# Performance work log

Measured on AMD Instinct MI355X. Metric: run time of the kernel, lower is better.

Reference implementation:

```python
import jax, jax.numpy as jnp
import numpy as np

WINDOW = 20  # local attention window, per create_sparse_mask


def _make_mask(rng, n, sparsity_ratio=0.1):
    # local band: |i - j| <= window//2 (covers start/end clamping and the diagonal)
    idx = jnp.arange(n)
    mask = jnp.abs(idx[:, None] - idx[None, :]) <= (WINDOW // 2)
    # random edges: n_random (i, j) pairs set to 1 (duplicates harmless)
    n_random = int(sparsity_ratio * n * n)
    k1, k2 = jax.random.split(rng)
    ri = jax.random.randint(k1, (n_random,), 0, n)
    rj = jax.random.randint(k2, (n_random,), 0, n)
    mask = mask.at[ri, rj].set(True)
    return mask  # [n, n] bool


def setup_inputs() -> dict:
    rng = jax.random.key(0)
    kq, kk, kv, km = jax.random.split(rng, 4)
    B, H, S, D = 1, 8, 4096, 32
    return {
        "query": jax.random.normal(kq, (B, H, S, D), dtype=jnp.float32),
        "key": jax.random.normal(kk, (B, H, S, D), dtype=jnp.float32),
        "value": jax.random.normal(kv, (B, H, S, D), dtype=jnp.float32),
        "mask": _make_mask(km, S, sparsity_ratio=0.1),
    }


def reference(query, key, value, mask):
    # query/key/value: [B, H, S, D]; mask: [S, S] bool (True = attend)
    head_dim = query.shape[-1]
    scale = 1.0 / jnp.sqrt(jnp.float32(head_dim))
    scores = jnp.einsum("bhqd,bhkd->bhqk", query, key) * scale
    # torch: scores = scores * mask; masked_fill(mask == 0, -inf) -> equivalent to where
    scores = jnp.where(mask[None, None, :, :], scores, -jnp.inf)
    attn = jax.nn.softmax(scores, axis=-1)
    attn = jnp.nan_to_num(attn, nan=0.0)
    return jnp.einsum("bhqk,bhkd->bhqd", attn, value)
```

## Files before the change

### kernel.cpp

```cpp
#include <hip/hip_runtime.h>
#include <hip/hip_bf16.h>


#define S_  4096
#define D_  32
#define H_  8

typedef _Float16 half8 __attribute__((ext_vector_type(8)));
typedef __fp16 fp16x2 __attribute__((ext_vector_type(2)));
typedef short short8 __attribute__((ext_vector_type(8)));
typedef short short4v __attribute__((ext_vector_type(4)));
typedef float float4v __attribute__((ext_vector_type(4)));
typedef unsigned short ushort_t;
typedef unsigned int u32;

#if __has_builtin(__builtin_amdgcn_exp2f)
#define EXP2(x) __builtin_amdgcn_exp2f(x)
#else
#define EXP2(x) exp2f(x)
#endif

__device__ inline ushort_t f2h(float x) {
    union { _Float16 h; ushort_t u; } c; c.h = (_Float16)x; return c.u;
}

__global__ __launch_bounds__(256)
void prep_qkv(const float* __restrict__ Q, const float* __restrict__ K,
              const float* __restrict__ V,
              ushort_t* __restrict__ Qh, ushort_t* __restrict__ Kt,
              ushort_t* __restrict__ Vt)
{
    const int bx = blockIdx.x;
    const int tid = threadIdx.x;
    union U8 { ushort_t u[8]; short8 v; };

    if (bx < 512) {
        const int e0 = (bx * 256 + tid) * 8;
        const float c = 0.17677669529663687f * 1.4426950408889634f;
        float4 a = *(const float4*)(Q + e0);
        float4 b = *(const float4*)(Q + e0 + 4);
        float f[8] = {a.x*c, a.y*c, a.z*c, a.w*c, b.x*c, b.y*c, b.z*c, b.w*c};
        U8 o;
#pragma unroll
        for (int i = 0; i < 8; ++i) o.u[i] = f2h(f[i]);
        *(short8*)(Qh + e0) = o.v;
    } else if (bx < 1024) {
        const int e0 = ((bx - 512) * 256 + tid) * 8;
        const int n = (e0 >> 3) & 15, quad = (e0 >> 7) & 3, t16 = (e0 >> 9) & 3;
        const int kt = (e0 >> 11) & 63, h = e0 >> 17;
        const int krow = kt * 64 + t16 * 16 + n;
        const float* src = K + ((size_t)h * S_ + krow) * D_ + quad * 8;
        float4 a = *(const float4*)src;
        float4 b = *(const float4*)(src + 4);
        float f[8] = {a.x, a.y, a.z, a.w, b.x, b.y, b.z, b.w};
        U8 o;
#pragma unroll
        for (int i = 0; i < 8; ++i) o.u[i] = f2h(f[i]);
        *(short8*)(Kt + e0) = o.v;
    } else {
        const int e0 = ((bx - 1024) * 256 + tid) * 8;
        const int n = (e0 >> 3) & 15, quad = (e0 >> 7) & 3;
        const int dhalf = (e0 >> 9) & 1, khalf = (e0 >> 10) & 1;
        const int kt = (e0 >> 11) & 63, h = e0 >> 17;
        const int d = dhalf * 16 + n;
        const int pbase = khalf * 32 + quad * 8;
        U8 o;
#pragma unroll
        for (int j = 0; j < 8; ++j) {
            int p = pbase + j;
            int krow = kt * 64 + (p & 3) * 16 + (p >> 2);
            o.u[j] = f2h(V[((size_t)h * S_ + krow) * D_ + d]);
        }
        *(short8*)(Vt + e0) = o.v;
    }
}

__global__ __launch_bounds__(256)
void prep_mask(const int* __restrict__ mask, ushort_t* __restrict__ mlane)
{
    __shared__ u32 msh[4096];
    const int tid = threadIdx.x;
    const int mb = blockIdx.x;
    const int qt16 = mb >> 2, cc = mb & 3;
#pragma unroll
    for (int i = 0; i < 16; ++i) {
        int4 m4 = *(const int4*)(mask + (size_t)(qt16 * 16 + i) * S_ + cc * 1024 + tid * 4);
        u32 v = (m4.x != 0 ? 1u : 0u) | (m4.y != 0 ? 0x100u : 0u)
              | (m4.z != 0 ? 0x10000u : 0u) | (m4.w != 0 ? 0x1000000u : 0u);
        msh[i * 256 + tid] = v;
    }
    __syncthreads();
    const int kt_local = tid >> 4, j = tid & 15;
    const int quad = j >> 2, n2 = j & 3;
    u32 o16[4] = {0, 0, 0, 0};
#pragma unroll
    for (int t16 = 0; t16 < 4; ++t16)
#pragma unroll
        for (int reg = 0; reg < 4; ++reg) {
            u32 v = msh[(quad * 4 + reg) * 256 + kt_local * 16 + t16 * 4 + n2];
            const int bp = t16 * 4 + reg;
            o16[0] |= (v & 1u) << bp;
            o16[1] |= ((v >> 8) & 1u) << bp;
            o16[2] |= ((v >> 16) & 1u) << bp;
            o16[3] |= ((v >> 24) & 1u) << bp;
        }
    union { u32 w[2]; short4v s; } pk;
    pk.w[0] = o16[0] | (o16[1] << 16);
    pk.w[1] = o16[2] | (o16[3] << 16);
    const int kt = cc * 16 + kt_local;
    *(short4v*)(mlane + ((size_t)(qt16 * 64 + kt) * 64 + j * 4)) = pk.s;
}


#define PS_STRIDE 72

__device__ inline void gl_lds16(const ushort_t* g, ushort_t* l) {
    __builtin_amdgcn_global_load_lds((const __attribute__((address_space(1))) void*)g,
                                     (__attribute__((address_space(3))) void*)l,
                                     16, 0, 0);
}

__global__ __launch_bounds__(512, 2)
void attn_mfma(const ushort_t* __restrict__ Qh, const ushort_t* __restrict__ Kt,
               const ushort_t* __restrict__ Vt, const ushort_t* __restrict__ mlane,
               float* __restrict__ out)
{
    __shared__ __align__(16) ushort_t sm[16384 + 8 * 16 * PS_STRIDE];
    ushort_t* K_s  = sm;
    ushort_t* Vt_s = sm + 8192;

    const int h  = blockIdx.y;
    const int q0 = blockIdx.x * 64;
    const int tid = threadIdx.x;
    const int w = tid >> 6, l = tid & 63;
    const int half = w >> 2, wl = w & 3;
    const int n16 = l & 15, quad = l >> 4;

    ushort_t* Ps = sm + 16384 + w * 16 * PS_STRIDE;

    const int qt16_u = __builtin_amdgcn_readfirstlane(blockIdx.x * 4 + wl);
    const ushort_t* mlw = mlane + ((size_t)qt16_u << 12);

    const int qrow = q0 + wl * 16 + n16;
    const half8 qh = *(const half8*)(Qh + ((size_t)h * S_ + qrow) * D_ + quad * 8);

    half8 ones;
#pragma unroll
    for (int i = 0; i < 8; ++i) ones[i] = (_Float16)1.0f;

    float4v o0 = {0.f, 0.f, 0.f, 0.f};
    float4v o1 = {0.f, 0.f, 0.f, 0.f};
    float4v lacc = {0.f, 0.f, 0.f, 0.f};

    const int hb = half * 4096;
    const int kt_base = half * 32;

    {
        const size_t tb = ((size_t)(h * 64 + kt_base)) * 2048 + wl * 512 + l * 8;
        gl_lds16(Kt + tb, K_s  + hb + wl * 512);
        gl_lds16(Vt + tb, Vt_s + hb + wl * 512);
    }
    __syncthreads();

    for (int i = 0; i < 32; ++i) {
        const int kt = kt_base + i;
        const int cb = hb + (i & 1) * 2048;
        if (i < 31) {
            const int nb = hb + ((i + 1) & 1) * 2048;
            const size_t tb = ((size_t)(h * 64 + kt + 1)) * 2048 + wl * 512 + l * 8;
            gl_lds16(Kt + tb, K_s  + nb + wl * 512);
            gl_lds16(Vt + tb, Vt_s + nb + wl * 512);
        }

        const u32 ml = mlw[kt * 64 + l];

        float pv[4][4];
#pragma unroll
        for (int t16 = 0; t16 < 4; ++t16) {
            const half8 kb = *(const half8*)(K_s + cb + (t16 * 4 + quad) * 128 + n16 * 8);
            float4v c = {0.f, 0.f, 0.f, 0.f};
            c = __builtin_amdgcn_mfma_f32_16x16x32_f16(qh, kb, c, 0, 0, 0);
#pragma unroll
            for (int reg = 0; reg < 4; ++reg) {
                float e = EXP2(c[reg]);
                pv[t16][reg] = (ml & (1u << (t16 * 4 + reg))) ? e : 0.f;
            }
        }
#pragma unroll
        for (int reg = 0; reg < 4; ++reg) {
            fp16x2 h01 = __builtin_amdgcn_cvt_pkrtz(pv[0][reg], pv[1][reg]);
            fp16x2 h23 = __builtin_amdgcn_cvt_pkrtz(pv[2][reg], pv[3][reg]);
            union { fp16x2 hh[2]; short4v s; } pk;
            pk.hh[0] = h01; pk.hh[1] = h23;
            *(short4v*)(Ps + (quad * 4 + reg) * PS_STRIDE + n16 * 4) = pk.s;
        }
        asm volatile("" ::: "memory");

#pragma unroll
        for (int khalf = 0; khalf < 2; ++khalf) {
            const half8 pa = *(const half8*)(Ps + n16 * PS_STRIDE + khalf * 32 + quad * 8);
            const half8 v0 = *(const half8*)(Vt_s + cb + ((khalf * 2 + 0) * 4 + quad) * 128 + n16 * 8);
            const half8 v1 = *(const half8*)(Vt_s + cb + ((khalf * 2 + 1) * 4 + quad) * 128 + n16 * 8);
            o0 = __builtin_amdgcn_mfma_f32_16x16x32_f16(pa, v0, o0, 0, 0, 0);
            o1 = __builtin_amdgcn_mfma_f32_16x16x32_f16(pa, v1, o1, 0, 0, 0);
            lacc = __builtin_amdgcn_mfma_f32_16x16x32_f16(pa, ones, lacc, 0, 0, 0);
        }

        __syncthreads();
    }

    float* red = (float*)sm;
    const int RSTR = 16 * 33 + 16;
    if (half == 1) {
        float* ro = red + wl * RSTR;
#pragma unroll
        for (int reg = 0; reg < 4; ++reg) {
            const int r = quad * 4 + reg;
            ro[r * 33 + n16]      = o0[reg];
            ro[r * 33 + 16 + n16] = o1[reg];
            if (n16 == 0) ro[16 * 33 + r] = lacc[reg];
        }
    }
    __syncthreads();
    if (half == 0) {
        const float* ro = red + wl * RSTR;
#pragma unroll
        for (int reg = 0; reg < 4; ++reg) {
            const int r = quad * 4 + reg;
            const float inv = 1.0f / (lacc[reg] + ro[16 * 33 + r]);
            const int row = q0 + wl * 16 + r;
            float* orow = out + ((size_t)h * S_ + row) * D_;
            orow[n16]      = (o0[reg] + ro[r * 33 + n16]) * inv;
            orow[16 + n16] = (o1[reg] + ro[r * 33 + 16 + n16]) * inv;
        }
    }
}


#define QT 64
#define KT 64
#define NSUB 4
#define KPT 16

__global__ __launch_bounds__(256, 2)
void sparse_attn_fp32(const float* __restrict__ Q, const float* __restrict__ K,
                      const float* __restrict__ V, const int* __restrict__ mask,
                      float* __restrict__ out)
{
    __shared__ float Ks[KT][D_];
    __shared__ float Vs[KT][D_];
    __shared__ float red_o[NSUB][QT][D_ + 1];
    __shared__ float red_l[NSUB][QT];

    const int h = blockIdx.y;
    const int q0 = blockIdx.x * QT;
    const int tid = threadIdx.x;
    const int ql = tid & 63;
    const int sub = tid >> 6;
    const int q = q0 + ql;
    const float scale = 0.17677669529663687f;

    float4 qreg[8];
    const float4* qrow = (const float4*)(Q + ((size_t)h * S_ + q) * D_);
#pragma unroll
    for (int i = 0; i < 8; ++i) qreg[i] = qrow[i];

    float o[D_];
#pragma unroll
    for (int d = 0; d < D_; ++d) o[d] = 0.f;
    float lsum0 = 0.f;

    const float* Kh = K + (size_t)h * S_ * D_;
    const float* Vh = V + (size_t)h * S_ * D_;

    for (int jt = 0; jt < S_; jt += KT) {
        __syncthreads();
        {
            const float4* gK = (const float4*)(Kh + (size_t)jt * D_);
            const float4* gV = (const float4*)(Vh + (size_t)jt * D_);
            float4* sK = (float4*)&Ks[0][0];
            float4* sV = (float4*)&Vs[0][0];
            sK[tid] = gK[tid]; sK[tid + 256] = gK[tid + 256];
            sV[tid] = gV[tid]; sV[tid + 256] = gV[tid + 256];
        }
        __syncthreads();

        int4 m4[4];
        {
            const int4* mr = (const int4*)(mask + (size_t)q * S_ + jt + sub * KPT);
#pragma unroll
            for (int i = 0; i < 4; ++i) m4[i] = mr[i];
        }
        const int* mb = (const int*)m4;

#pragma unroll
        for (int kk = 0; kk < KPT; ++kk) {
            const int jl = sub * KPT + kk;
            const float4* krow = (const float4*)&Ks[jl][0];
            float s = 0.f;
#pragma unroll
            for (int i = 0; i < 8; ++i) {
                float4 kv = krow[i];
                s += qreg[i].x * kv.x + qreg[i].y * kv.y + qreg[i].z * kv.z + qreg[i].w * kv.w;
            }
            const float p = mb[kk] ? __expf(s * scale) : 0.f;
            lsum0 += p;
            const float4* vrow = (const float4*)&Vs[jl][0];
#pragma unroll
            for (int i = 0; i < 8; ++i) {
                float4 vv = vrow[i];
                o[i * 4 + 0] += p * vv.x;
                o[i * 4 + 1] += p * vv.y;
                o[i * 4 + 2] += p * vv.z;
                o[i * 4 + 3] += p * vv.w;
            }
        }
    }

#pragma unroll
    for (int d = 0; d < D_; ++d) red_o[sub][ql][d] = o[d];
    red_l[sub][ql] = lsum0;
    __syncthreads();

    const int eq = tid & 63;
    const int dg = tid >> 6;
    float acc[8];
#pragma unroll
    for (int i = 0; i < 8; ++i) acc[i] = 0.f;
    float lsum = 0.f;
#pragma unroll
    for (int s2 = 0; s2 < NSUB; ++s2) {
        lsum += red_l[s2][eq];
#pragma unroll
        for (int i = 0; i < 8; ++i) acc[i] += red_o[s2][eq][dg * 8 + i];
    }
    const float inv = 1.0f / lsum;
    float* orow = out + ((size_t)h * S_ + q0 + eq) * D_ + dg * 8;
#pragma unroll
    for (int i = 0; i < 8; ++i) orow[i] = acc[i] * inv;
}


extern "C" void kernel_launch(void* const* d_in, const int* in_sizes, int n_in,
                              void* d_out, int out_size, void* d_ws, size_t ws_size,
                              hipStream_t stream) {
    const float* Q = (const float*)d_in[0];
    const float* K = (const float*)d_in[1];
    const float* V = (const float*)d_in[2];
    const int* mask = (const int*)d_in[3];
    float* out = (float*)d_out;

    const size_t MB = 1024 * 1024;
    if (ws_size < 8 * MB) {
        dim3 grid(S_ / QT, H_);
        sparse_attn_fp32<<<grid, 256, 0, stream>>>(Q, K, V, mask, out);
        return;
    }

    char* ws = (char*)d_ws;
    ushort_t* Qh = (ushort_t*)(ws + 0 * MB);
    ushort_t* Kt = (ushort_t*)(ws + 2 * MB);
    ushort_t* Vt = (ushort_t*)(ws + 4 * MB);
    ushort_t* mlane = (ushort_t*)(ws + 6 * MB);

    prep_qkv<<<1536, 256, 0, stream>>>(Q, K, V, Qh, Kt, Vt);
    prep_mask<<<1024, 256, 0, stream>>>(mask, mlane);

    dim3 grid(S_ / 64, H_);
    attn_mfma<<<grid, 512, 0, stream>>>(Qh, Kt, Vt, mlane, out);
}
```

Baseline: 143.1 us.

## Process two 16-row query tiles per wave to reuse K/V LDS reads

The attention kernel drops from 8 waves to 4 waves per block, and each wave now computes two 16-row query tiles (A and B) against the same K/V fragments read from LDS. Each K and V fragment load therefore feeds twice as many MFMAs, and each wave issues more global-to-LDS copies per tile. Per-wave register use roughly doubles and there are fewer waves available to hide latency. The block still covers 64 query rows, so the grid is unchanged.

```diff
diff --git a/kernel.cpp b/kernel.cpp
--- a/kernel.cpp
+++ b/kernel.cpp
@@ -120,12 +120,12 @@
                                      16, 0, 0);
 }
 
-__global__ __launch_bounds__(512, 2)
+__global__ __launch_bounds__(256, 2)
 void attn_mfma(const ushort_t* __restrict__ Qh, const ushort_t* __restrict__ Kt,
                const ushort_t* __restrict__ Vt, const ushort_t* __restrict__ mlane,
                float* __restrict__ out)
 {
-    __shared__ __align__(16) ushort_t sm[16384 + 8 * 16 * PS_STRIDE];
+    __shared__ __align__(16) ushort_t sm[16384 + 4 * 32 * PS_STRIDE];
     ushort_t* K_s  = sm;
     ushort_t* Vt_s = sm + 8192;
 
@@ -133,32 +133,35 @@
     const int q0 = blockIdx.x * 64;
     const int tid = threadIdx.x;
     const int w = tid >> 6, l = tid & 63;
-    const int half = w >> 2, wl = w & 3;
+    const int g = w & 1, hf = w >> 1;
     const int n16 = l & 15, quad = l >> 4;
 
-    ushort_t* Ps = sm + 16384 + w * 16 * PS_STRIDE;
-
-    const int qt16_u = __builtin_amdgcn_readfirstlane(blockIdx.x * 4 + wl);
-    const ushort_t* mlw = mlane + ((size_t)qt16_u << 12);
-
-    const int qrow = q0 + wl * 16 + n16;
-    const half8 qh = *(const half8*)(Qh + ((size_t)h * S_ + qrow) * D_ + quad * 8);
+    ushort_t* Ps = sm + 16384 + w * 32 * PS_STRIDE;
+
+    const int qt16A = __builtin_amdgcn_readfirstlane(blockIdx.x * 4 + g * 2);
+    const ushort_t* mlwA = mlane + ((size_t)qt16A << 12);
+    const ushort_t* mlwB = mlane + ((size_t)(qt16A + 1) << 12);
+
+    const int qA = q0 + g * 32 + n16;
+    const half8 qhA = *(const half8*)(Qh + ((size_t)h * S_ + qA) * D_ + quad * 8);
+    const half8 qhB = *(const half8*)(Qh + ((size_t)h * S_ + qA + 16) * D_ + quad * 8);
 
     half8 ones;
 #pragma unroll
     for (int i = 0; i < 8; ++i) ones[i] = (_Float16)1.0f;
 
-    float4v o0 = {0.f, 0.f, 0.f, 0.f};
-    float4v o1 = {0.f, 0.f, 0.f, 0.f};
-    float4v lacc = {0.f, 0.f, 0.f, 0.f};
-
-    const int hb = half * 4096;
-    const int kt_base = half * 32;
+    float4v o0A = {0,0,0,0}, o1A = {0,0,0,0}, lA = {0,0,0,0};
+    float4v o0B = {0,0,0,0}, o1B = {0,0,0,0}, lB = {0,0,0,0};
+
+    const int hb = hf * 4096;
+    const int kt_base = hf * 32;
 
     {
-        const size_t tb = ((size_t)(h * 64 + kt_base)) * 2048 + wl * 512 + l * 8;
-        gl_lds16(Kt + tb, K_s  + hb + wl * 512);
-        gl_lds16(Vt + tb, Vt_s + hb + wl * 512);
+        const size_t tb = ((size_t)(h * 64 + kt_base)) * 2048 + g * 1024 + l * 8;
+        gl_lds16(Kt + tb,       K_s  + hb + g * 1024 + l * 8);
+        gl_lds16(Kt + tb + 512, K_s  + hb + g * 1024 + 512 + l * 8);
+        gl_lds16(Vt + tb,       Vt_s + hb + g * 1024 + l * 8);
+        gl_lds16(Vt + tb + 512, Vt_s + hb + g * 1024 + 512 + l * 8);
     }
     __syncthreads();
 
@@ -167,71 +170,94 @@
         const int cb = hb + (i & 1) * 2048;
         if (i < 31) {
             const int nb = hb + ((i + 1) & 1) * 2048;
-            const size_t tb = ((size_t)(h * 64 + kt + 1)) * 2048 + wl * 512 + l * 8;
-            gl_lds16(Kt + tb, K_s  + nb + wl * 512);
-            gl_lds16(Vt + tb, Vt_s + nb + wl * 512);
-        }
-
-        const u32 ml = mlw[kt * 64 + l];
-
-        float pv[4][4];
+            const size_t tb = ((size_t)(h * 64 + kt + 1)) * 2048 + g * 1024 + l * 8;
+            gl_lds16(Kt + tb,       K_s  + nb + g * 1024 + l * 8);
+            gl_lds16(Kt + tb + 512, K_s  + nb + g * 1024 + 512 + l * 8);
+            gl_lds16(Vt + tb,       Vt_s + nb + g * 1024 + l * 8);
+            gl_lds16(Vt + tb + 512, Vt_s + nb + g * 1024 + 512 + l * 8);
+        }
+
+        const u32 mlA = mlwA[kt * 64 + l];
+        const u32 mlB = mlwB[kt * 64 + l];
+
+        float pvA[4][4], pvB[4][4];
 #pragma unroll
         for (int t16 = 0; t16 < 4; ++t16) {
             const half8 kb = *(const half8*)(K_s + cb + (t16 * 4 + quad) * 128 + n16 * 8);
-            float4v c = {0.f, 0.f, 0.f, 0.f};
-            c = __builtin_amdgcn_mfma_f32_16x16x32_f16(qh, kb, c, 0, 0, 0);
+            float4v cA = {0,0,0,0}, cB = {0,0,0,0};
+            cA = __builtin_amdgcn_mfma_f32_16x16x32_f16(qhA, kb, cA, 0, 0, 0);
+            cB = __builtin_amdgcn_mfma_f32_16x16x32_f16(qhB, kb, cB, 0, 0, 0);
 #pragma unroll
             for (int reg = 0; reg < 4; ++reg) {
-                float e = EXP2(c[reg]);
-                pv[t16][reg] = (ml & (1u << (t16 * 4 + reg))) ? e : 0.f;
+                float eA = EXP2(cA[reg]);
+                float eB = EXP2(cB[reg]);
+                pvA[t16][reg] = (mlA & (1u << (t16 * 4 + reg))) ? eA : 0.f;
+                pvB[t16][reg] = (mlB & (1u << (t16 * 4 + reg))) ? eB : 0.f;
             }
         }
 #pragma unroll
         for (int reg = 0; reg < 4; ++reg) {
-            fp16x2 h01 = __builtin_amdgcn_cvt_pkrtz(pv[0][reg], pv[1][reg]);
-            fp16x2 h23 = __builtin_amdgcn_cvt_pkrtz(pv[2][reg], pv[3][reg]);
-            union { fp16x2 hh[2]; short4v s; } pk;
-            pk.hh[0] = h01; pk.hh[1] = h23;
-            *(short4v*)(Ps + (quad * 4 + reg) * PS_STRIDE + n16 * 4) = pk.s;
+            fp16x2 a01 = __builtin_amdgcn_cvt_pkrtz(pvA[0][reg], pvA[1][reg]);
+            fp16x2 a23 = __builtin_amdgcn_cvt_pkrtz(pvA[2][reg], pvA[3][reg]);
+            union { fp16x2 hh[2]; short4v s; } pkA;
+            pkA.hh[0] = a01; pkA.hh[1] = a23;
+            *(short4v*)(Ps + (quad * 4 + reg) * PS_STRIDE + n16 * 4) = pkA.s;
+            fp16x2 b01 = __builtin_amdgcn_cvt_pkrtz(pvB[0][reg], pvB[1][reg]);
+            fp16x2 b23 = __builtin_amdgcn_cvt_pkrtz(pvB[2][reg], pvB[3][reg]);
+            union { fp16x2 hh[2]; short4v s; } pkB;
+            pkB.hh[0] = b01; pkB.hh[1] = b23;
+            *(short4v*)(Ps + (16 + quad * 4 + reg) * PS_STRIDE + n16 * 4) = pkB.s;
         }
         asm volatile("" ::: "memory");
 
 #pragma unroll
         for (int khalf = 0; khalf < 2; ++khalf) {
-            const half8 pa = *(const half8*)(Ps + n16 * PS_STRIDE + khalf * 32 + quad * 8);
+            const half8 paA = *(const half8*)(Ps + n16 * PS_STRIDE + khalf * 32 + quad * 8);
+            const half8 paB = *(const half8*)(Ps + (16 + n16) * PS_STRIDE + khalf * 32 + quad * 8);
             const half8 v0 = *(const half8*)(Vt_s + cb + ((khalf * 2 + 0) * 4 + quad) * 128 + n16 * 8);
             const half8 v1 = *(const half8*)(Vt_s + cb + ((khalf * 2 + 1) * 4 + quad) * 128 + n16 * 8);
-            o0 = __builtin_amdgcn_mfma_f32_16x16x32_f16(pa, v0, o0, 0, 0, 0);
-            o1 = __builtin_amdgcn_mfma_f32_16x16x32_f16(pa, v1, o1, 0, 0, 0);
-            lacc = __builtin_amdgcn_mfma_f32_16x16x32_f16(pa, ones, lacc, 0, 0, 0);
+            o0A = __builtin_amdgcn_mfma_f32_16x16x32_f16(paA, v0, o0A, 0, 0, 0);
+            o1A = __builtin_amdgcn_mfma_f32_16x16x32_f16(paA, v1, o1A, 0, 0, 0);
+            lA  = __builtin_amdgcn_mfma_f32_16x16x32_f16(paA, ones, lA, 0, 0, 0);
+            o0B = __builtin_amdgcn_mfma_f32_16x16x32_f16(paB, v0, o0B, 0, 0, 0);
+            o1B = __builtin_amdgcn_mfma_f32_16x16x32_f16(paB, v1, o1B, 0, 0, 0);
+            lB  = __builtin_amdgcn_mfma_f32_16x16x32_f16(paB, ones, lB, 0, 0, 0);
         }
 
         __syncthreads();
     }
 
     float* red = (float*)sm;
-    const int RSTR = 16 * 33 + 16;
-    if (half == 1) {
-        float* ro = red + wl * RSTR;
+    const int RSTR = 32 * 33 + 32;
+    if (hf == 1) {
+        float* ro = red + g * RSTR;
 #pragma unroll
         for (int reg = 0; reg < 4; ++reg) {
-            const int r = quad * 4 + reg;
-            ro[r * 33 + n16]      = o0[reg];
-            ro[r * 33 + 16 + n16] = o1[reg];
-            if (n16 == 0) ro[16 * 33 + r] = lacc[reg];
+            const int rA = quad * 4 + reg, rB = 16 + rA;
+            ro[rA * 33 + n16]      = o0A[reg];
+            ro[rA * 33 + 16 + n16] = o1A[reg];
+            ro[rB * 33 + n16]      = o0B[reg];
+            ro[rB * 33 + 16 + n16] = o1B[reg];
+            if (n16 == 0) {
+                ro[32 * 33 + rA] = lA[reg];
+                ro[32 * 33 + rB] = lB[reg];
+            }
         }
     }
     __syncthreads();
-    if (half == 0) {
-        const float* ro = red + wl * RSTR;
+    if (hf == 0) {
+        const float* ro = red + g * RSTR;
 #pragma unroll
         for (int reg = 0; reg < 4; ++reg) {
-            const int r = quad * 4 + reg;
-            const float inv = 1.0f / (lacc[reg] + ro[16 * 33 + r]);
-            const int row = q0 + wl * 16 + r;
-            float* orow = out + ((size_t)h * S_ + row) * D_;
-            orow[n16]      = (o0[reg] + ro[r * 33 + n16]) * inv;
-            orow[16 + n16] = (o1[reg] + ro[r * 33 + 16 + n16]) * inv;
+            const int rA = quad * 4 + reg, rB = 16 + rA;
+            const float invA = 1.0f / (lA[reg] + ro[32 * 33 + rA]);
+            const float invB = 1.0f / (lB[reg] + ro[32 * 33 + rB]);
+            float* orA = out + ((size_t)h * S_ + q0 + g * 32 + rA) * D_;
+            float* orB = out + ((size_t)h * S_ + q0 + g * 32 + rB) * D_;
+            orA[n16]      = (o0A[reg] + ro[rA * 33 + n16]) * invA;
+            orA[16 + n16] = (o1A[reg] + ro[rA * 33 + 16 + n16]) * invA;
+            orB[n16]      = (o0B[reg] + ro[rB * 33 + n16]) * invB;
+            orB[16 + n16] = (o1B[reg] + ro[rB * 33 + 16 + n16]) * invB;
         }
     }
 }
@@ -367,5 +393,5 @@
     prep_mask<<<1024, 256, 0, stream>>>(mask, mlane);
 
     dim3 grid(S_ / 64, H_);
-    attn_mfma<<<grid, 512, 0, stream>>>(Qh, Kt, Vt, mlane, out);
-}
+    attn_mfma<<<grid, 256, 0, stream>>>(Qh, Kt, Vt, mlane, out);
+}
```

Result: slower. 147.5 us (+3.1%).

## Fuse fp32-to-fp16 QKV conversion into attention kernel and drop prep pass

Applied to the files above, without the earlier changes.

Removes the separate prep_qkv kernel and the fp16 workspace copies of Q, K and V. The attention kernel now loads fp32 Q/K/V directly, scales and converts Q in registers, and loads each K/V tile into registers one iteration ahead. It converts and stores those tiles to LDS after the PV MFMAs, replacing the async global-to-LDS loads. This saves a launch and a global write/read round-trip, at the cost of reading twice the bytes per tile, strided scalar V gathers, and more register pressure in the inner loop.

```diff
diff --git a/kernel.cpp b/kernel.cpp
--- a/kernel.cpp
+++ b/kernel.cpp
@@ -20,61 +20,6 @@
 #define EXP2(x) exp2f(x)
 #endif
 
-__device__ inline ushort_t f2h(float x) {
-    union { _Float16 h; ushort_t u; } c; c.h = (_Float16)x; return c.u;
-}
-
-__global__ __launch_bounds__(256)
-void prep_qkv(const float* __restrict__ Q, const float* __restrict__ K,
-              const float* __restrict__ V,
-              ushort_t* __restrict__ Qh, ushort_t* __restrict__ Kt,
-              ushort_t* __restrict__ Vt)
-{
-    const int bx = blockIdx.x;
-    const int tid = threadIdx.x;
-    union U8 { ushort_t u[8]; short8 v; };
-
-    if (bx < 512) {
-        const int e0 = (bx * 256 + tid) * 8;
-        const float c = 0.17677669529663687f * 1.4426950408889634f;
-        float4 a = *(const float4*)(Q + e0);
-        float4 b = *(const float4*)(Q + e0 + 4);
-        float f[8] = {a.x*c, a.y*c, a.z*c, a.w*c, b.x*c, b.y*c, b.z*c, b.w*c};
-        U8 o;
-#pragma unroll
-        for (int i = 0; i < 8; ++i) o.u[i] = f2h(f[i]);
-        *(short8*)(Qh + e0) = o.v;
-    } else if (bx < 1024) {
-        const int e0 = ((bx - 512) * 256 + tid) * 8;
-        const int n = (e0 >> 3) & 15, quad = (e0 >> 7) & 3, t16 = (e0 >> 9) & 3;
-        const int kt = (e0 >> 11) & 63, h = e0 >> 17;
-        const int krow = kt * 64 + t16 * 16 + n;
-        const float* src = K + ((size_t)h * S_ + krow) * D_ + quad * 8;
-        float4 a = *(const float4*)src;
-        float4 b = *(const float4*)(src + 4);
-        float f[8] = {a.x, a.y, a.z, a.w, b.x, b.y, b.z, b.w};
-        U8 o;
-#pragma unroll
-        for (int i = 0; i < 8; ++i) o.u[i] = f2h(f[i]);
-        *(short8*)(Kt + e0) = o.v;
-    } else {
-        const int e0 = ((bx - 1024) * 256 + tid) * 8;
-        const int n = (e0 >> 3) & 15, quad = (e0 >> 7) & 3;
-        const int dhalf = (e0 >> 9) & 1, khalf = (e0 >> 10) & 1;
-        const int kt = (e0 >> 11) & 63, h = e0 >> 17;
-        const int d = dhalf * 16 + n;
-        const int pbase = khalf * 32 + quad * 8;
-        U8 o;
-#pragma unroll
-        for (int j = 0; j < 8; ++j) {
-            int p = pbase + j;
-            int krow = kt * 64 + (p & 3) * 16 + (p >> 2);
-            o.u[j] = f2h(V[((size_t)h * S_ + krow) * D_ + d]);
-        }
-        *(short8*)(Vt + e0) = o.v;
-    }
-}
-
 __global__ __launch_bounds__(256)
 void prep_mask(const int* __restrict__ mask, ushort_t* __restrict__ mlane)
 {
@@ -114,15 +59,9 @@
 
 #define PS_STRIDE 72
 
-__device__ inline void gl_lds16(const ushort_t* g, ushort_t* l) {
-    __builtin_amdgcn_global_load_lds((const __attribute__((address_space(1))) void*)g,
-                                     (__attribute__((address_space(3))) void*)l,
-                                     16, 0, 0);
-}
-
 __global__ __launch_bounds__(512, 2)
-void attn_mfma(const ushort_t* __restrict__ Qh, const ushort_t* __restrict__ Kt,
-               const ushort_t* __restrict__ Vt, const ushort_t* __restrict__ mlane,
+void attn_mfma(const float* __restrict__ Qf, const float* __restrict__ Kf,
+               const float* __restrict__ Vf, const ushort_t* __restrict__ mlane,
                float* __restrict__ out)
 {
     __shared__ __align__(16) ushort_t sm[16384 + 8 * 16 * PS_STRIDE];
@@ -135,6 +74,7 @@
     const int w = tid >> 6, l = tid & 63;
     const int half = w >> 2, wl = w & 3;
     const int n16 = l & 15, quad = l >> 4;
+    const int khalf = (wl >> 1) & 1, dhalf = wl & 1;
 
     ushort_t* Ps = sm + 16384 + w * 16 * PS_STRIDE;
 
@@ -142,7 +82,15 @@
     const ushort_t* mlw = mlane + ((size_t)qt16_u << 12);
 
     const int qrow = q0 + wl * 16 + n16;
-    const half8 qh = *(const half8*)(Qh + ((size_t)h * S_ + qrow) * D_ + quad * 8);
+    const float* qp = Qf + ((size_t)h * S_ + qrow) * D_ + quad * 8;
+    const float4 qa = *(const float4*)qp;
+    const float4 qb = *(const float4*)(qp + 4);
+    const float c = 0.17677669529663687f * 1.4426950408889634f;
+    half8 qh;
+    qh[0] = (_Float16)(qa.x * c); qh[1] = (_Float16)(qa.y * c);
+    qh[2] = (_Float16)(qa.z * c); qh[3] = (_Float16)(qa.w * c);
+    qh[4] = (_Float16)(qb.x * c); qh[5] = (_Float16)(qb.y * c);
+    qh[6] = (_Float16)(qb.z * c); qh[7] = (_Float16)(qb.w * c);
 
     half8 ones;
 #pragma unroll
@@ -155,22 +103,48 @@
     const int hb = half * 4096;
     const int kt_base = half * 32;
 
-    {
-        const size_t tb = ((size_t)(h * 64 + kt_base)) * 2048 + wl * 512 + l * 8;
-        gl_lds16(Kt + tb, K_s  + hb + wl * 512);
-        gl_lds16(Vt + tb, Vt_s + hb + wl * 512);
-    }
+    float4 ka, kb4;
+    float vv[8];
+    const float* Kh = Kf + (size_t)h * S_ * D_;
+    const float* Vh = Vf + (size_t)h * S_ * D_;
+    const int vd = dhalf * 16 + n16;
+
+#define LOAD_TILE(ktv)                                                        \
+    {                                                                         \
+        const float* kp = Kh + ((size_t)((ktv) * 64 + wl * 16 + n16)) * D_ + quad * 8; \
+        ka  = *(const float4*)kp;                                             \
+        kb4 = *(const float4*)(kp + 4);                                       \
+        _Pragma("unroll")                                                     \
+        for (int j = 0; j < 8; ++j) {                                         \
+            const int krow = (ktv) * 64 + (j & 3) * 16 + khalf * 8 + quad * 2 + (j >> 2); \
+            vv[j] = Vh[(size_t)krow * D_ + vd];                               \
+        }                                                                     \
+    }
+
+#define STORE_TILE(bufv)                                                      \
+    {                                                                         \
+        union { fp16x2 hh[4]; short8 s; } pk;                                 \
+        pk.hh[0] = __builtin_amdgcn_cvt_pkrtz(ka.x, ka.y);                    \
+        pk.hh[1] = __builtin_amdgcn_cvt_pkrtz(ka.z, ka.w);                    \
+        pk.hh[2] = __builtin_amdgcn_cvt_pkrtz(kb4.x, kb4.y);                  \
+        pk.hh[3] = __builtin_amdgcn_cvt_pkrtz(kb4.z, kb4.w);                  \
+        *(short8*)(K_s + hb + (bufv) * 2048 + wl * 512 + l * 8) = pk.s;       \
+        union { fp16x2 hh[4]; short8 s; } pv2;                                \
+        pv2.hh[0] = __builtin_amdgcn_cvt_pkrtz(vv[0], vv[1]);                 \
+        pv2.hh[1] = __builtin_amdgcn_cvt_pkrtz(vv[2], vv[3]);                 \
+        pv2.hh[2] = __builtin_amdgcn_cvt_pkrtz(vv[4], vv[5]);                 \
+        pv2.hh[3] = __builtin_amdgcn_cvt_pkrtz(vv[6], vv[7]);                 \
+        *(short8*)(Vt_s + hb + (bufv) * 2048 + wl * 512 + l * 8) = pv2.s;     \
+    }
+
+    LOAD_TILE(kt_base);
+    STORE_TILE(0);
     __syncthreads();
 
     for (int i = 0; i < 32; ++i) {
         const int kt = kt_base + i;
         const int cb = hb + (i & 1) * 2048;
-        if (i < 31) {
-            const int nb = hb + ((i + 1) & 1) * 2048;
-            const size_t tb = ((size_t)(h * 64 + kt + 1)) * 2048 + wl * 512 + l * 8;
-            gl_lds16(Kt + tb, K_s  + nb + wl * 512);
-            gl_lds16(Vt + tb, Vt_s + nb + wl * 512);
-        }
+        if (i < 31) LOAD_TILE(kt + 1);
 
         const u32 ml = mlw[kt * 64 + l];
 
@@ -178,11 +152,11 @@
 #pragma unroll
         for (int t16 = 0; t16 < 4; ++t16) {
             const half8 kb = *(const half8*)(K_s + cb + (t16 * 4 + quad) * 128 + n16 * 8);
-            float4v c = {0.f, 0.f, 0.f, 0.f};
-            c = __builtin_amdgcn_mfma_f32_16x16x32_f16(qh, kb, c, 0, 0, 0);
+            float4v cc = {0.f, 0.f, 0.f, 0.f};
+            cc = __builtin_amdgcn_mfma_f32_16x16x32_f16(qh, kb, cc, 0, 0, 0);
 #pragma unroll
             for (int reg = 0; reg < 4; ++reg) {
-                float e = EXP2(c[reg]);
+                float e = EXP2(cc[reg]);
                 pv[t16][reg] = (ml & (1u << (t16 * 4 + reg))) ? e : 0.f;
             }
         }
@@ -197,14 +171,16 @@
         asm volatile("" ::: "memory");
 
 #pragma unroll
-        for (int khalf = 0; khalf < 2; ++khalf) {
-            const half8 pa = *(const half8*)(Ps + n16 * PS_STRIDE + khalf * 32 + quad * 8);
-            const half8 v0 = *(const half8*)(Vt_s + cb + ((khalf * 2 + 0) * 4 + quad) * 128 + n16 * 8);
-            const half8 v1 = *(const half8*)(Vt_s + cb + ((khalf * 2 + 1) * 4 + quad) * 128 + n16 * 8);
+        for (int khf = 0; khf < 2; ++khf) {
+            const half8 pa = *(const half8*)(Ps + n16 * PS_STRIDE + khf * 32 + quad * 8);
+            const half8 v0 = *(const half8*)(Vt_s + cb + ((khf * 2 + 0) * 4 + quad) * 128 + n16 * 8);
+            const half8 v1 = *(const half8*)(Vt_s + cb + ((khf * 2 + 1) * 4 + quad) * 128 + n16 * 8);
             o0 = __builtin_amdgcn_mfma_f32_16x16x32_f16(pa, v0, o0, 0, 0, 0);
             o1 = __builtin_amdgcn_mfma_f32_16x16x32_f16(pa, v1, o1, 0, 0, 0);
             lacc = __builtin_amdgcn_mfma_f32_16x16x32_f16(pa, ones, lacc, 0, 0, 0);
         }
+
+        if (i < 31) STORE_TILE((i + 1) & 1);
 
         __syncthreads();
     }
@@ -234,6 +210,8 @@
             orow[16 + n16] = (o1[reg] + ro[r * 33 + 16 + n16]) * inv;
         }
     }
+#undef LOAD_TILE
+#undef STORE_TILE
 }
 
 
@@ -351,21 +329,16 @@
     float* out = (float*)d_out;
 
     const size_t MB = 1024 * 1024;
-    if (ws_size < 8 * MB) {
+    if (ws_size < 2 * MB) {
         dim3 grid(S_ / QT, H_);
         sparse_attn_fp32<<<grid, 256, 0, stream>>>(Q, K, V, mask, out);
         return;
     }
 
-    char* ws = (char*)d_ws;
-    ushort_t* Qh = (ushort_t*)(ws + 0 * MB);
-    ushort_t* Kt = (ushort_t*)(ws + 2 * MB);
-    ushort_t* Vt = (ushort_t*)(ws + 4 * MB);
-    ushort_t* mlane = (ushort_t*)(ws + 6 * MB);
-
-    prep_qkv<<<1536, 256, 0, stream>>>(Q, K, V, Qh, Kt, Vt);
+    ushort_t* mlane = (ushort_t*)d_ws;
+
     prep_mask<<<1024, 256, 0, stream>>>(mask, mlane);
 
     dim3 grid(S_ / 64, H_);
-    attn_mfma<<<grid, 512, 0, stream>>>(Qh, Kt, Vt, mlane, out);
+    attn_mfma<<<grid, 512, 0, stream>>>(Q, K, V, mlane, out);
 }
```

After: 152.5 us. 6.6% more time.

## Fuse prep and attention kernels into one cooperative launch with grid sync

Applied to the files above, without the earlier changes.

Merges the QKV conversion, mask bit-packing and MFMA attention into a single cooperative kernel, using a grid-wide sync between the prep phase and the attention phase. The aim is to remove two extra kernel launches and the gaps between them. In exchange it depends on cooperative launch support and on all 512 blocks of 512 threads being co-resident (two per CU). It also adds a device-attribute query on the host at every call, and falls back to the three-kernel path if the cooperative launch fails.

```diff
diff --git a/kernel.cpp b/kernel.cpp
--- a/kernel.cpp
+++ b/kernel.cpp
@@ -1,6 +1,9 @@
 #include <hip/hip_runtime.h>
 #include <hip/hip_bf16.h>
-
+#include <hip/hip_cooperative_groups.h>
+
+
+namespace cg = cooperative_groups;
 
 #define S_  4096
 #define D_  32
@@ -23,6 +26,222 @@
 __device__ inline ushort_t f2h(float x) {
     union { _Float16 h; ushort_t u; } c; c.h = (_Float16)x; return c.u;
 }
+
+#define PS_STRIDE 72
+
+__device__ inline void gl_lds16(const ushort_t* g, ushort_t* l) {
+    __builtin_amdgcn_global_load_lds((const __attribute__((address_space(1))) void*)g,
+                                     (__attribute__((address_space(3))) void*)l,
+                                     16, 0, 0);
+}
+
+__global__ __launch_bounds__(512, 2)
+void attn_all(const float* __restrict__ Qf, const float* __restrict__ Kf,
+              const float* __restrict__ Vf, const int* __restrict__ mask,
+              ushort_t* __restrict__ Qh, ushort_t* __restrict__ Kt,
+              ushort_t* __restrict__ Vt, ushort_t* __restrict__ mlane,
+              float* __restrict__ out)
+{
+    __shared__ __align__(16) ushort_t sm[16384 + 8 * 16 * PS_STRIDE];
+
+    const int tid = threadIdx.x;
+    const int blockid = blockIdx.y * 64 + blockIdx.x;
+
+    {
+        const int sub = tid >> 8, stid = tid & 255;
+        union U8 { ushort_t u[8]; short8 v; };
+#pragma unroll
+        for (int pass = 0; pass < 2; ++pass) {
+            const int vb = blockid * 2 + sub + pass * 1024;
+            if (vb < 512) {
+                const int e0 = (vb * 256 + stid) * 8;
+                const float c = 0.17677669529663687f * 1.4426950408889634f;
+                float4 a = *(const float4*)(Qf + e0);
+                float4 b = *(const float4*)(Qf + e0 + 4);
+                float f[8] = {a.x*c, a.y*c, a.z*c, a.w*c, b.x*c, b.y*c, b.z*c, b.w*c};
+                U8 o;
+#pragma unroll
+                for (int i = 0; i < 8; ++i) o.u[i] = f2h(f[i]);
+                *(short8*)(Qh + e0) = o.v;
+            } else if (vb < 1024) {
+                const int e0 = ((vb - 512) * 256 + stid) * 8;
+                const int n = (e0 >> 3) & 15, quad = (e0 >> 7) & 3, t16 = (e0 >> 9) & 3;
+                const int kt = (e0 >> 11) & 63, h = e0 >> 17;
+                const int krow = kt * 64 + t16 * 16 + n;
+                const float* src = Kf + ((size_t)h * S_ + krow) * D_ + quad * 8;
+                float4 a = *(const float4*)src;
+                float4 b = *(const float4*)(src + 4);
+                float f[8] = {a.x, a.y, a.z, a.w, b.x, b.y, b.z, b.w};
+                U8 o;
+#pragma unroll
+                for (int i = 0; i < 8; ++i) o.u[i] = f2h(f[i]);
+                *(short8*)(Kt + e0) = o.v;
+            } else if (vb < 1536) {
+                const int e0 = ((vb - 1024) * 256 + stid) * 8;
+                const int n = (e0 >> 3) & 15, quad = (e0 >> 7) & 3;
+                const int dhalf = (e0 >> 9) & 1, khalf = (e0 >> 10) & 1;
+                const int kt = (e0 >> 11) & 63, h = e0 >> 17;
+                const int d = dhalf * 16 + n;
+                const int pbase = khalf * 32 + quad * 8;
+                U8 o;
+#pragma unroll
+                for (int j = 0; j < 8; ++j) {
+                    int p = pbase + j;
+                    int krow = kt * 64 + (p & 3) * 16 + (p >> 2);
+                    o.u[j] = f2h(Vf[((size_t)h * S_ + krow) * D_ + d]);
+                }
+                *(short8*)(Vt + e0) = o.v;
+            }
+        }
+    }
+
+    {
+        u32* msh = (u32*)sm;
+        const int sub = tid >> 8, stid = tid & 255;
+        u32* m0 = msh + sub * 4096;
+        const int mb = blockid * 2 + sub;
+        const int qt16 = mb >> 2, cc = mb & 3;
+#pragma unroll
+        for (int i = 0; i < 16; ++i) {
+            int4 m4 = *(const int4*)(mask + (size_t)(qt16 * 16 + i) * S_ + cc * 1024 + stid * 4);
+            u32 v = (m4.x != 0 ? 1u : 0u) | (m4.y != 0 ? 0x100u : 0u)
+                  | (m4.z != 0 ? 0x10000u : 0u) | (m4.w != 0 ? 0x1000000u : 0u);
+            m0[i * 256 + stid] = v;
+        }
+        __syncthreads();
+        const int kt_local = stid >> 4, j = stid & 15;
+        const int quad = j >> 2, n2 = j & 3;
+        u32 o16[4] = {0, 0, 0, 0};
+#pragma unroll
+        for (int t16 = 0; t16 < 4; ++t16)
+#pragma unroll
+            for (int reg = 0; reg < 4; ++reg) {
+                u32 v = m0[(quad * 4 + reg) * 256 + kt_local * 16 + t16 * 4 + n2];
+                const int bp = t16 * 4 + reg;
+                o16[0] |= (v & 1u) << bp;
+                o16[1] |= ((v >> 8) & 1u) << bp;
+                o16[2] |= ((v >> 16) & 1u) << bp;
+                o16[3] |= ((v >> 24) & 1u) << bp;
+            }
+        union { u32 w[2]; short4v s; } pk;
+        pk.w[0] = o16[0] | (o16[1] << 16);
+        pk.w[1] = o16[2] | (o16[3] << 16);
+        const int kt = cc * 16 + kt_local;
+        *(short4v*)(mlane + ((size_t)(qt16 * 64 + kt) * 64 + j * 4)) = pk.s;
+    }
+
+    __threadfence();
+    cg::this_grid().sync();
+
+    ushort_t* K_s  = sm;
+    ushort_t* Vt_s = sm + 8192;
+
+    const int h  = blockIdx.y;
+    const int q0 = blockIdx.x * 64;
+    const int w = tid >> 6, l = tid & 63;
+    const int half = w >> 2, wl = w & 3;
+    const int n16 = l & 15, quad = l >> 4;
+
+    ushort_t* Ps = sm + 16384 + w * 16 * PS_STRIDE;
+
+    const int qt16_u = __builtin_amdgcn_readfirstlane(blockIdx.x * 4 + wl);
+    const ushort_t* mlw = mlane + ((size_t)qt16_u << 12);
+
+    const int qrow = q0 + wl * 16 + n16;
+    const half8 qh = *(const half8*)(Qh + ((size_t)h * S_ + qrow) * D_ + quad * 8);
+
+    half8 ones;
+#pragma unroll
+    for (int i = 0; i < 8; ++i) ones[i] = (_Float16)1.0f;
+
+    float4v o0 = {0.f, 0.f, 0.f, 0.f};
+    float4v o1 = {0.f, 0.f, 0.f, 0.f};
+    float4v lacc = {0.f, 0.f, 0.f, 0.f};
+
+    const int hb = half * 4096;
+    const int kt_base = half * 32;
+
+    {
+        const size_t tb = ((size_t)(h * 64 + kt_base)) * 2048 + wl * 512 + l * 8;
+        gl_lds16(Kt + tb, K_s  + hb + wl * 512);
+        gl_lds16(Vt + tb, Vt_s + hb + wl * 512);
+    }
+    __syncthreads();
+
+    for (int i = 0; i < 32; ++i) {
+        const int kt = kt_base + i;
+        const int cb = hb + (i & 1) * 2048;
+        if (i < 31) {
+            const int nb = hb + ((i + 1) & 1) * 2048;
+            const size_t tb = ((size_t)(h * 64 + kt + 1)) * 2048 + wl * 512 + l * 8;
+            gl_lds16(Kt + tb, K_s  + nb + wl * 512);
+            gl_lds16(Vt + tb, Vt_s + nb + wl * 512);
+        }
+
+        const u32 ml = mlw[kt * 64 + l];
+
+        float pv[4][4];
+#pragma unroll
+        for (int t16 = 0; t16 < 4; ++t16) {
+            const half8 kb = *(const half8*)(K_s + cb + (t16 * 4 + quad) * 128 + n16 * 8);
+            float4v c = {0.f, 0.f, 0.f, 0.f};
+            c = __builtin_amdgcn_mfma_f32_16x16x32_f16(qh, kb, c, 0, 0, 0);
+#pragma unroll
+            for (int reg = 0; reg < 4; ++reg) {
+                float e = EXP2(c[reg]);
+                pv[t16][reg] = (ml & (1u << (t16 * 4 + reg))) ? e : 0.f;
+            }
+        }
+#pragma unroll
+        for (int reg = 0; reg < 4; ++reg) {
+            fp16x2 h01 = __builtin_amdgcn_cvt_pkrtz(pv[0][reg], pv[1][reg]);
+            fp16x2 h23 = __builtin_amdgcn_cvt_pkrtz(pv[2][reg], pv[3][reg]);
+            union { fp16x2 hh[2]; short4v s; } pk;
+            pk.hh[0] = h01; pk.hh[1] = h23;
+            *(short4v*)(Ps + (quad * 4 + reg) * PS_STRIDE + n16 * 4) = pk.s;
+        }
+        asm volatile("" ::: "memory");
+
+#pragma unroll
+        for (int khalf = 0; khalf < 2; ++khalf) {
+            const half8 pa = *(const half8*)(Ps + n16 * PS_STRIDE + khalf * 32 + quad * 8);
+            const half8 v0 = *(const half8*)(Vt_s + cb + ((khalf * 2 + 0) * 4 + quad) * 128 + n16 * 8);
+            const half8 v1 = *(const half8*)(Vt_s + cb + ((khalf * 2 + 1) * 4 + quad) * 128 + n16 * 8);
+            o0 = __builtin_amdgcn_mfma_f32_16x16x32_f16(pa, v0, o0, 0, 0, 0);
+            o1 = __builtin_amdgcn_mfma_f32_16x16x32_f16(pa, v1, o1, 0, 0, 0);
+            lacc = __builtin_amdgcn_mfma_f32_16x16x32_f16(pa, ones, lacc, 0, 0, 0);
+        }
+
+        __syncthreads();
+    }
+
+    float* red = (float*)sm;
+    const int RSTR = 16 * 33 + 16;
+    if (half == 1) {
+        float* ro = red + wl * RSTR;
+#pragma unroll
+        for (int reg = 0; reg < 4; ++reg) {
+            const int r = quad * 4 + reg;
+            ro[r * 33 + n16]      = o0[reg];
+            ro[r * 33 + 16 + n16] = o1[reg];
+            if (n16 == 0) ro[16 * 33 + r] = lacc[reg];
+        }
+    }
+    __syncthreads();
+    if (half == 0) {
+        const float* ro = red + wl * RSTR;
+#pragma unroll
+        for (int reg = 0; reg < 4; ++reg) {
+            const int r = quad * 4 + reg;
+            const float inv = 1.0f / (lacc[reg] + ro[16 * 33 + r]);
+            const int row = q0 + wl * 16 + r;
+            float* orow = out + ((size_t)h * S_ + row) * D_;
+            orow[n16]      = (o0[reg] + ro[r * 33 + n16]) * inv;
+            orow[16 + n16] = (o1[reg] + ro[r * 33 + 16 + n16]) * inv;
+        }
+    }
+}
+
 
 __global__ __launch_bounds__(256)
 void prep_qkv(const float* __restrict__ Q, const float* __restrict__ K,
@@ -33,7 +252,6 @@
     const int bx = blockIdx.x;
     const int tid = threadIdx.x;
     union U8 { ushort_t u[8]; short8 v; };
-
     if (bx < 512) {
         const int e0 = (bx * 256 + tid) * 8;
         const float c = 0.17677669529663687f * 1.4426950408889634f;
@@ -111,15 +329,6 @@
     *(short4v*)(mlane + ((size_t)(qt16 * 64 + kt) * 64 + j * 4)) = pk.s;
 }
 
-
-#define PS_STRIDE 72
-
-__device__ inline void gl_lds16(const ushort_t* g, ushort_t* l) {
-    __builtin_amdgcn_global_load_lds((const __attribute__((address_space(1))) void*)g,
-                                     (__attribute__((address_space(3))) void*)l,
-                                     16, 0, 0);
-}
-
 __global__ __launch_bounds__(512, 2)
 void attn_mfma(const ushort_t* __restrict__ Qh, const ushort_t* __restrict__ Kt,
                const ushort_t* __restrict__ Vt, const ushort_t* __restrict__ mlane,
@@ -137,7 +346,6 @@
     const int n16 = l & 15, quad = l >> 4;
 
     ushort_t* Ps = sm + 16384 + w * 16 * PS_STRIDE;
-
     const int qt16_u = __builtin_amdgcn_readfirstlane(blockIdx.x * 4 + wl);
     const ushort_t* mlw = mlane + ((size_t)qt16_u << 12);
 
@@ -154,7 +362,6 @@
 
     const int hb = half * 4096;
     const int kt_base = half * 32;
-
     {
         const size_t tb = ((size_t)(h * 64 + kt_base)) * 2048 + wl * 512 + l * 8;
         gl_lds16(Kt + tb, K_s  + hb + wl * 512);
@@ -171,9 +378,7 @@
             gl_lds16(Kt + tb, K_s  + nb + wl * 512);
             gl_lds16(Vt + tb, Vt_s + nb + wl * 512);
         }
-
         const u32 ml = mlw[kt * 64 + l];
-
         float pv[4][4];
 #pragma unroll
         for (int t16 = 0; t16 < 4; ++t16) {
@@ -195,7 +400,6 @@
             *(short4v*)(Ps + (quad * 4 + reg) * PS_STRIDE + n16 * 4) = pk.s;
         }
         asm volatile("" ::: "memory");
-
 #pragma unroll
         for (int khalf = 0; khalf < 2; ++khalf) {
             const half8 pa = *(const half8*)(Ps + n16 * PS_STRIDE + khalf * 32 + quad * 8);
@@ -205,7 +409,6 @@
             o1 = __builtin_amdgcn_mfma_f32_16x16x32_f16(pa, v1, o1, 0, 0, 0);
             lacc = __builtin_amdgcn_mfma_f32_16x16x32_f16(pa, ones, lacc, 0, 0, 0);
         }
-
         __syncthreads();
     }
 
@@ -363,9 +566,22 @@
     ushort_t* Vt = (ushort_t*)(ws + 4 * MB);
     ushort_t* mlane = (ushort_t*)(ws + 6 * MB);
 
+    int coop = 0;
+    hipDeviceGetAttribute(&coop, hipDeviceAttributeCooperativeLaunch, 0);
+
+    if (coop) {
+        dim3 grid(S_ / 64, H_);
+        dim3 block(512);
+        void* args[] = {(void*)&Q, (void*)&K, (void*)&V, (void*)&mask,
+                        (void*)&Qh, (void*)&Kt, (void*)&Vt, (void*)&mlane,
+                        (void*)&out};
+        hipError_t err = hipLaunchCooperativeKernel((const void*)attn_all, grid, block,
+                                                    args, 0, stream);
+        if (err == hipSuccess) return;
+    }
+
     prep_qkv<<<1536, 256, 0, stream>>>(Q, K, V, Qh, Kt, Vt);
     prep_mask<<<1024, 256, 0, stream>>>(mask, mlane);
-
     dim3 grid(S_ / 64, H_);
     attn_mfma<<<grid, 512, 0, stream>>>(Qh, Kt, Vt, mlane, out);
 }
```

Measured after the change: 317.6 us. +122.0%, slower.
